# Kernel tuning notes

Hardware: AMD Instinct MI355X
Metric: run time of the kernel (lower is better)

The kernel has to match this reference:

```python
import math
import jax, jax.numpy as jnp
import numpy as np

B, N, D, E, DN, H, M = 32, 64, 256, 32, 64, 8, 32
EPS = 1e-5


def _ln(x):
    # param-free layer norm over the last axis
    mu = jnp.mean(x, axis=-1, keepdims=True)
    var = jnp.var(x, axis=-1, keepdims=True)
    return (x - mu) * jax.lax.rsqrt(var + EPS)


def setup_inputs() -> dict:
    key = jax.random.key(0)
    ks = jax.random.split(key, 9)
    embeddings = jax.random.normal(ks[0], (B, N, D), dtype=jnp.float32)
    edge_features = jax.random.normal(ks[1], (B, N, N, E), dtype=jnp.float32)
    mask = jax.random.randint(ks[2], (B, N), 0, 2).astype(bool)
    node_features = jax.random.normal(ks[3], (B, N, DN), dtype=jnp.float32)
    s = lambda d: 1.0 / math.sqrt(d)
    W_edge = jax.random.normal(ks[4], (E, H, M), dtype=jnp.float32) * s(E)
    W_recv = jax.random.normal(ks[5], (D, H, M), dtype=jnp.float32) * s(D)
    W_send = jax.random.normal(ks[6], (D, H, M), dtype=jnp.float32) * s(D)
    W_recv_node = jax.random.normal(ks[7], (DN, H, M), dtype=jnp.float32) * s(DN)
    W_send_node = jax.random.normal(ks[8], (DN, H, M), dtype=jnp.float32) * s(DN)
    return dict(embeddings=embeddings, edge_features=edge_features, mask=mask,
                node_features=node_features, W_edge=W_edge, W_recv=W_recv,
                W_send=W_send, W_recv_node=W_recv_node, W_send_node=W_send_node)


def reference(embeddings, edge_features, mask, node_features,
              W_edge, W_recv, W_send, W_recv_node, W_send_node):
    sqrt2 = math.sqrt(2.0)
    mask_f = mask.astype(embeddings.dtype)  # [B, N]
    emb = _ln(embeddings) * mask_f[..., None]  # [B, N, D]
    # double mask: [B, sender, receiver, 1]
    dm = (mask_f[..., None, :, None] * mask_f[..., :, None, None])
    ef = edge_features * dm  # [B, N, N, E]
    # projections to (heads, message_dim)
    edge_part = jnp.einsum('bije,ehm->bijhm', ef, W_edge)        # [B,N,N,H,M]
    recv = jnp.einsum('bjd,dhm->bjhm', emb, W_recv) / sqrt2      # [B,N,H,M]
    send = jnp.einsum('bid,dhm->bihm', emb, W_send) / sqrt2
    # receiver broadcast over sender axis (-4), sender over receiver axis (-3)
    rs = jnp.tanh(recv[..., None, :, :, :] + send[..., :, None, :, :])  # [B,N,N,H,M]
    rn = jnp.einsum('bjd,dhm->bjhm', node_features, W_recv_node)
    sn = jnp.einsum('bid,dhm->bihm', node_features, W_send_node)
    rs = rs * jax.nn.sigmoid((rn[..., None, :, :, :] + sn[..., :, None, :, :]) / sqrt2)
    msgs = rs * edge_part * dm[..., None]  # [B,N,N,H,M]
    updates = msgs.sum(axis=-4)            # sum over senders -> [B,N,H,M]
    updates = _ln(updates)
    return jnp.reshape(updates, (*updates.shape[:-2], -1))  # [B,N,H*M]
```

## Files before the change

kernel.cpp:

```cpp
#include <hip/hip_runtime.h>
#include <hip/hip_bf16.h>
#include <math.h>

#define B_   32
#define N_   64
#define D_   256
#define E_   32
#define DN_  64
#define H_   8
#define M_   32
#define HM_  256
#define BN_  2048
#define EPS_ 1e-5f
#define SQRT2_    1.41421356237309515f
#define NINVSQ2_ (-0.70710678118654752f)
#define MAGIC_ 0x5EEDCAFEF00DBEEFULL

typedef float f32x4 __attribute__((ext_vector_type(4)));
typedef short bf16x8 __attribute__((ext_vector_type(8)));
union U4S8 { uint4 u; bf16x8 s; };
union F2U  { float2 f; unsigned long long u; };

__device__ __forceinline__ unsigned pk2(float a, float b) {
    union { __hip_bfloat162 h; unsigned u; } cv;
    cv.h = __float22bfloat162_rn(make_float2(a, b));
    return cv.u;
}


__global__ __launch_bounds__(256, 2) void one_k(
        const float* __restrict__ emb, const float* __restrict__ edge,
        const int* __restrict__ mraw, const float* __restrict__ nfeat,
        const float* __restrict__ We, const float* __restrict__ Wr,
        const float* __restrict__ Ws, const float* __restrict__ Wrn,
        const float* __restrict__ Wsn, float* __restrict__ out,
        unsigned long long* __restrict__ g_rr,
        unsigned long long* __restrict__ g_ssC,
        unsigned long long* __restrict__ flags)
{
    const int t = threadIdx.x;
    const int w = t >> 6, l = t & 63, hi = l >> 4, lo = l & 15;
    const int blk = blockIdx.x, b = blk >> 4, s = blk & 15;
    const int j0 = s * 4;

    __shared__ int s_flag, cnt_sh;
    __shared__ unsigned long long bits_sh;
    __shared__ int sidx_s[N_];
    __shared__ __align__(16) unsigned short eln[64 * 256];
    __shared__ __align__(16) unsigned short nfs[64 * 64];
    __shared__ __align__(16) uint4 ldsA[4][256];

    if (t == 0) s_flag = 0;
    __syncthreads();
    { int v0 = mraw[t], v1 = mraw[t + 256];
      if (((v0 | v1) & ~1) != 0) atomicOr(&s_flag, 1); }
    __syncthreads();
    const bool bytef = (s_flag != 0);
    const unsigned char* mbb = (const unsigned char*)mraw;
    if (w == 0) {
        const int k = b * N_ + l;
        const bool on = bytef ? (mbb[k] != 0) : (mraw[k] != 0);
        unsigned long long bits = __ballot(on);
        if (l == 0) { bits_sh = bits; cnt_sh = __popcll(bits); }
        int p = __popcll(bits & ((1ull << l) - 1ull));
        if (on) sidx_s[p] = l;
        if (l >= __popcll(bits)) sidx_s[l] = -1;
    }
    __syncthreads();
    const unsigned long long bits = bits_sh;
    const int cb = cnt_sh;

    {
        const int mt = t >> 6, phi = (t >> 4) & 3, plo = t & 15;
        const int si = sidx_s[mt * 16 + plo];
        if (si >= 0) {
            const float* rb = edge + ((size_t)((b * N_ + si) * N_ + j0)) * E_ + phi * 8;
            #pragma unroll
            for (int q = 0; q < 4; ++q) {
                float4 v0 = *(const float4*)(rb + q * E_);
                float4 v1 = *(const float4*)(rb + q * E_ + 4);
                ldsA[q][t] = make_uint4(pk2(v0.x, v0.y), pk2(v0.z, v0.w),
                                        pk2(v1.x, v1.y), pk2(v1.z, v1.w));
            }
        } else {
            #pragma unroll
            for (int q = 0; q < 4; ++q) ldsA[q][t] = make_uint4(0, 0, 0, 0);
        }
    }

    for (int rr2 = 0; rr2 < 16; ++rr2) {
        const int i = w * 16 + rr2;
        const float mfv = ((bits >> i) & 1ull) ? 1.0f : 0.0f;
        float4 x = *(const float4*)(emb + (size_t)(b * N_ + i) * D_ + l * 4);
        float ssum = x.x + x.y + x.z + x.w;
        float s2 = x.x*x.x + x.y*x.y + x.z*x.z + x.w*x.w;
        #pragma unroll
        for (int k = 32; k >= 1; k >>= 1) { ssum += __shfl_xor(ssum, k); s2 += __shfl_xor(s2, k); }
        float mu  = ssum * (1.0f / D_);
        float var = s2 * (1.0f / D_) - mu * mu;
        float rs  = rsqrtf(var + EPS_) * mfv;
        unsigned p0 = pk2((x.x - mu) * rs, (x.y - mu) * rs);
        unsigned p1 = pk2((x.z - mu) * rs, (x.w - mu) * rs);
        unsigned off = (unsigned)(i * 512) + (((unsigned)(l * 8)) ^ (((unsigned)(i & 15)) << 4));
        *(uint2*)((char*)eln + off) = make_uint2(p0, p1);
    }
    #pragma unroll
    for (int it = 0; it < 4; ++it) {
        const int idx = it * 1024 + t * 4;
        const int r = idx >> 6, cc = idx & 63;
        float4 x = *(const float4*)(nfeat + (size_t)(b * N_ + r) * DN_ + cc);
        unsigned off = (unsigned)(r * 128) + (((unsigned)(cc * 2)) ^ (((unsigned)(r & 7)) << 4));
        *(uint2*)((char*)nfs + off) = make_uint2(pk2(x.x, x.y), pk2(x.z, x.w));
    }
    __syncthreads();

    const int nb = s * 16 + lo;
    f32x4 aR = {0,0,0,0}, aS = {0,0,0,0}, aRN = {0,0,0,0}, aSN = {0,0,0,0};
    #pragma unroll
    for (int ks = 0; ks < 8; ++ks) {
        const int i = w * 16 + lo;
        U4S8 a; a.u = *(const uint4*)((const char*)eln +
                      (unsigned)(i * 512) + (((unsigned)(ks * 64 + hi * 16)) ^ (((unsigned)(i & 15)) << 4)));
        const float* wrp = Wr + (size_t)(ks * 32 + hi * 8) * HM_ + nb;
        const float* wsp = Ws + (size_t)(ks * 32 + hi * 8) * HM_ + nb;
        U4S8 br, bs;
        br.u = make_uint4(pk2(wrp[0],     wrp[HM_]),    pk2(wrp[2*HM_], wrp[3*HM_]),
                          pk2(wrp[4*HM_], wrp[5*HM_]),  pk2(wrp[6*HM_], wrp[7*HM_]));
        bs.u = make_uint4(pk2(wsp[0],     wsp[HM_]),    pk2(wsp[2*HM_], wsp[3*HM_]),
                          pk2(wsp[4*HM_], wsp[5*HM_]),  pk2(wsp[6*HM_], wsp[7*HM_]));
        aR = __builtin_amdgcn_mfma_f32_16x16x32_bf16(a.s, br.s, aR, 0, 0, 0);
        aS = __builtin_amdgcn_mfma_f32_16x16x32_bf16(a.s, bs.s, aS, 0, 0, 0);
        if (ks < 2) {
            U4S8 a2; a2.u = *(const uint4*)((const char*)nfs +
                          (unsigned)(i * 128) + (((unsigned)(ks * 64 + hi * 16)) ^ (((unsigned)(i & 7)) << 4)));
            const float* wrn = Wrn + (size_t)(ks * 32 + hi * 8) * HM_ + nb;
            const float* wsn = Wsn + (size_t)(ks * 32 + hi * 8) * HM_ + nb;
            U4S8 brn, bsn;
            brn.u = make_uint4(pk2(wrn[0],     wrn[HM_]),   pk2(wrn[2*HM_], wrn[3*HM_]),
                               pk2(wrn[4*HM_], wrn[5*HM_]), pk2(wrn[6*HM_], wrn[7*HM_]));
            bsn.u = make_uint4(pk2(wsn[0],     wsn[HM_]),   pk2(wsn[2*HM_], wsn[3*HM_]),
                               pk2(wsn[4*HM_], wsn[5*HM_]), pk2(wsn[6*HM_], wsn[7*HM_]));
            aRN = __builtin_amdgcn_mfma_f32_16x16x32_bf16(a2.s, brn.s, aRN, 0, 0, 0);
            aSN = __builtin_amdgcn_mfma_f32_16x16x32_bf16(a2.s, bsn.s, aSN, 0, 0, 0);
        }
    }
    #pragma unroll
    for (int r = 0; r < 4; ++r) {
        const int i = w * 16 + hi * 4 + r;
        F2U rrv; rrv.f = make_float2(__expf(SQRT2_ * aR[r]), __expf(NINVSQ2_ * aRN[r]));
        __hip_atomic_store(&g_rr[(size_t)(b * N_ + i) * HM_ + nb], rrv.u,
                           __ATOMIC_RELAXED, __HIP_MEMORY_SCOPE_AGENT);
        if ((bits >> i) & 1ull) {
            const int p = __popcll(bits & ((1ull << i) - 1ull));
            F2U sv; sv.f = make_float2(__expf(SQRT2_ * aS[r]), __expf(NINVSQ2_ * aSN[r]));
            __hip_atomic_store(&g_ssC[(size_t)(b * N_ + p) * HM_ + nb], sv.u,
                               __ATOMIC_RELAXED, __HIP_MEMORY_SCOPE_AGENT);
        }
    }
    for (int p = cb + (t >> 4); p < N_; p += 16)
        __hip_atomic_store(&g_ssC[(size_t)(b * N_ + p) * HM_ + s * 16 + (t & 15)], 0ull,
                           __ATOMIC_RELAXED, __HIP_MEMORY_SCOPE_AGENT);
    __syncthreads();
    if (t == 0)
        __hip_atomic_store(&flags[b * 16 + s], MAGIC_,
                           __ATOMIC_RELEASE, __HIP_MEMORY_SCOPE_AGENT);

    if (t < 16) {
        int guard = 100000;
        while (guard-- > 0 &&
               __hip_atomic_load(&flags[b * 16 + t],
                                 __ATOMIC_ACQUIRE, __HIP_MEMORY_SCOPE_AGENT) != MAGIC_) {}
    }
    __syncthreads();

    U4S8 b4[4];
    #pragma unroll
    for (int nl = 0; nl < 4; ++nl) {
        const float* wp = We + (size_t)(hi * 8) * HM_ + w * 64 + nl * 16 + lo;
        b4[nl].u = make_uint4(pk2(wp[0],     wp[HM_]),    pk2(wp[2*HM_], wp[3*HM_]),
                              pk2(wp[4*HM_], wp[5*HM_]),  pk2(wp[6*HM_], wp[7*HM_]));
    }
    F2U rrq[4][4];
    #pragma unroll
    for (int q = 0; q < 4; ++q)
        #pragma unroll
        for (int nl = 0; nl < 4; ++nl)
            rrq[q][nl].u = __hip_atomic_load(
                &g_rr[(size_t)(b * N_ + j0 + q) * HM_ + w * 64 + nl * 16 + lo],
                __ATOMIC_RELAXED, __HIP_MEMORY_SCOPE_AGENT);

    float upd[4][4];
    #pragma unroll
    for (int q = 0; q < 4; ++q)
        #pragma unroll
        for (int nl = 0; nl < 4; ++nl) upd[q][nl] = 0.0f;

    const f32x4 zero = {0.0f, 0.0f, 0.0f, 0.0f};
    #pragma unroll
    for (int mt = 0; mt < 4; ++mt) {
        if (mt * 16 < cb) {
            F2U ssv[4][4];
            #pragma unroll
            for (int r = 0; r < 4; ++r)
                #pragma unroll
                for (int nl = 0; nl < 4; ++nl)
                    ssv[r][nl].u = __hip_atomic_load(
                        &g_ssC[(size_t)(b * N_ + mt * 16 + hi * 4 + r) * HM_ + w * 64 + nl * 16 + lo],
                        __ATOMIC_RELAXED, __HIP_MEMORY_SCOPE_AGENT);
            #pragma unroll
            for (int q = 0; q < 4; ++q) {
                if ((bits >> (j0 + q)) & 1ull) {
                    U4S8 a; a.u = ldsA[q][mt * 64 + l];
                    f32x4 acc[4];
                    #pragma unroll
                    for (int nl = 0; nl < 4; ++nl)
                        acc[nl] = __builtin_amdgcn_mfma_f32_16x16x32_bf16(a.s, b4[nl].s, zero, 0, 0, 0);
                    #pragma unroll
                    for (int r = 0; r < 4; ++r)
                        #pragma unroll
                        for (int nl = 0; nl < 4; ++nl) {
                            float u = rrq[q][nl].f.x * ssv[r][nl].f.x;
                            float v = rrq[q][nl].f.y * ssv[r][nl].f.y;
                            float den = (u + 1.0f) * (v + 1.0f);
                            float g = (u - 1.0f) * __builtin_amdgcn_rcpf(den);
                            upd[q][nl] = fmaf(g, acc[nl][r], upd[q][nl]);
                        }
                }
            }
        }
    }
    #pragma unroll
    for (int q = 0; q < 4; ++q) {
        const int j = j0 + q, bn = b * N_ + j;
        if (!((bits >> j) & 1ull)) {
            out[(size_t)bn * HM_ + w * 64 + l] = 0.0f;
            continue;
        }
        float u0 = upd[q][0], u1 = upd[q][1], u2 = upd[q][2], u3 = upd[q][3];
        u0 += __shfl_xor(u0, 16); u0 += __shfl_xor(u0, 32);
        u1 += __shfl_xor(u1, 16); u1 += __shfl_xor(u1, 32);
        u2 += __shfl_xor(u2, 16); u2 += __shfl_xor(u2, 32);
        u3 += __shfl_xor(u3, 16); u3 += __shfl_xor(u3, 32);
        float s0 = u0 + u1, q0 = u0*u0 + u1*u1;
        float s1 = u2 + u3, q1 = u2*u2 + u3*u3;
        #pragma unroll
        for (int k = 8; k >= 1; k >>= 1) {
            s0 += __shfl_xor(s0, k); q0 += __shfl_xor(q0, k);
            s1 += __shfl_xor(s1, k); q1 += __shfl_xor(q1, k);
        }
        float mu0 = s0 * (1.0f / M_), va0 = q0 * (1.0f / M_) - mu0 * mu0;
        float mu1 = s1 * (1.0f / M_), va1 = q1 * (1.0f / M_) - mu1 * mu1;
        float rs0 = rsqrtf(va0 + EPS_), rs1 = rsqrtf(va1 + EPS_);
        float v01 = (hi & 1) ? u1 : u0;
        float v23 = (hi & 1) ? u3 : u2;
        float val = (hi < 2) ? v01 : v23;
        float o = (hi < 2) ? (val - mu0) * rs0 : (val - mu1) * rs1;
        out[(size_t)bn * HM_ + w * 64 + l] = o;
    }
}

extern "C" void kernel_launch(void* const* d_in, const int* in_sizes, int n_in,
                              void* d_out, int out_size, void* d_ws, size_t ws_size,
                              hipStream_t stream) {
    const float* embeddings = (const float*)d_in[0];
    const float* edge_feat  = (const float*)d_in[1];
    const int*   mask_raw   = (const int*)d_in[2];
    const float* node_feat  = (const float*)d_in[3];
    const float* W_edge     = (const float*)d_in[4];
    const float* W_recv     = (const float*)d_in[5];
    const float* W_send     = (const float*)d_in[6];
    const float* W_recvn    = (const float*)d_in[7];
    const float* W_sendn    = (const float*)d_in[8];
    float* out = (float*)d_out;

    unsigned long long* g_ssC = (unsigned long long*)d_ws;
    unsigned long long* g_rr  = g_ssC + (size_t)BN_ * HM_;
    unsigned long long* flags = g_rr + (size_t)BN_ * HM_;

    one_k<<<512, 256, 0, stream>>>(embeddings, edge_feat, mask_raw, node_feat,
                                   W_edge, W_recv, W_send, W_recvn, W_sendn,
                                   out, g_rr, g_ssC, flags);
}
```

Measured before the change: 41.82 us.

## Split fused kernel into node and edge kernels, drop flag spin-wait

Replaces the single fused kernel, which used inter-block spin-waiting on global flags, with two launches. The node kernel computes the projections, applies layer norm directly from registers without staging in LDS, and writes through plain stores instead of atomics. The edge kernel consumes those results after the launch boundary and exits early when all four receivers in its tile are masked. It also remaps blocks by XCD so each batch's blocks share an L2, adds an occupancy hint of 4, and trims LDS use; the cost is a second launch and its gap.

```diff
diff --git a/kernel.cpp b/kernel.cpp
--- a/kernel.cpp
+++ b/kernel.cpp
@@ -14,12 +14,10 @@
 #define EPS_ 1e-5f
 #define SQRT2_    1.41421356237309515f
 #define NINVSQ2_ (-0.70710678118654752f)
-#define MAGIC_ 0x5EEDCAFEF00DBEEFULL
 
 typedef float f32x4 __attribute__((ext_vector_type(4)));
 typedef short bf16x8 __attribute__((ext_vector_type(8)));
 union U4S8 { uint4 u; bf16x8 s; };
-union F2U  { float2 f; unsigned long long u; };
 
 __device__ __forceinline__ unsigned pk2(float a, float b) {
     union { __hip_bfloat162 h; unsigned u; } cv;
@@ -28,47 +26,153 @@
 }
 
 
-__global__ __launch_bounds__(256, 2) void one_k(
-        const float* __restrict__ emb, const float* __restrict__ edge,
-        const int* __restrict__ mraw, const float* __restrict__ nfeat,
-        const float* __restrict__ We, const float* __restrict__ Wr,
-        const float* __restrict__ Ws, const float* __restrict__ Wrn,
-        const float* __restrict__ Wsn, float* __restrict__ out,
-        unsigned long long* __restrict__ g_rr,
-        unsigned long long* __restrict__ g_ssC,
-        unsigned long long* __restrict__ flags)
-{
-    const int t = threadIdx.x;
-    const int w = t >> 6, l = t & 63, hi = l >> 4, lo = l & 15;
-    const int blk = blockIdx.x, b = blk >> 4, s = blk & 15;
-    const int j0 = s * 4;
-
-    __shared__ int s_flag, cnt_sh;
-    __shared__ unsigned long long bits_sh;
-    __shared__ int sidx_s[N_];
-    __shared__ __align__(16) unsigned short eln[64 * 256];
-    __shared__ __align__(16) unsigned short nfs[64 * 64];
-    __shared__ __align__(16) uint4 ldsA[4][256];
-
-    if (t == 0) s_flag = 0;
+__device__ __forceinline__ void remap(int wg, int& b, int& s) {
+    const int xcd = wg & 7;
+    b = xcd * 4 + (wg >> 7);
+    s = (wg >> 3) & 15;
+}
+
+__device__ __forceinline__ unsigned long long mask_bits(
+        const int* mraw, int b, int t, int w, int l, int* s_flag_sh,
+        unsigned long long* bits_sh) {
+    if (t == 0) *s_flag_sh = 0;
     __syncthreads();
     { int v0 = mraw[t], v1 = mraw[t + 256];
-      if (((v0 | v1) & ~1) != 0) atomicOr(&s_flag, 1); }
-    __syncthreads();
-    const bool bytef = (s_flag != 0);
+      if (((v0 | v1) & ~1) != 0) atomicOr(s_flag_sh, 1); }
+    __syncthreads();
+    const bool bytef = (*s_flag_sh != 0);
     const unsigned char* mbb = (const unsigned char*)mraw;
     if (w == 0) {
         const int k = b * N_ + l;
         const bool on = bytef ? (mbb[k] != 0) : (mraw[k] != 0);
         unsigned long long bits = __ballot(on);
-        if (l == 0) { bits_sh = bits; cnt_sh = __popcll(bits); }
+        if (l == 0) *bits_sh = bits;
+    }
+    __syncthreads();
+    return *bits_sh;
+}
+
+__global__ __launch_bounds__(256, 4) void node_k(
+        const float* __restrict__ emb, const float* __restrict__ nfeat,
+        const int* __restrict__ mraw,
+        const float* __restrict__ Wr, const float* __restrict__ Ws,
+        const float* __restrict__ Wrn, const float* __restrict__ Wsn,
+        float2* __restrict__ g_rr, float2* __restrict__ g_ssC) {
+    const int t = threadIdx.x;
+    const int w = t >> 6, l = t & 63, hi = l >> 4, lo = l & 15;
+    int b, s; remap(blockIdx.x, b, s);
+
+    __shared__ int s_flag;
+    __shared__ unsigned long long bits_sh;
+    const unsigned long long bits = mask_bits(mraw, b, t, w, l, &s_flag, &bits_sh);
+    const int cb = __popcll(bits);
+
+    float mu_l, rs_l;
+    {
+        const int qrow = w * 16 + (l >> 2);
+        const float* rp = emb + (size_t)(b * N_ + qrow) * D_ + (l & 3) * 64;
+        float sv = 0.f, s2 = 0.f;
+        #pragma unroll
+        for (int k = 0; k < 16; ++k) {
+            float4 x = *(const float4*)(rp + k * 4);
+            sv += x.x + x.y + x.z + x.w;
+            s2 += x.x*x.x + x.y*x.y + x.z*x.z + x.w*x.w;
+        }
+        sv += __shfl_xor(sv, 1); sv += __shfl_xor(sv, 2);
+        s2 += __shfl_xor(s2, 1); s2 += __shfl_xor(s2, 2);
+        float mu  = sv * (1.0f / D_);
+        float var = s2 * (1.0f / D_) - mu * mu;
+        float rs  = rsqrtf(var + EPS_) * (((bits >> qrow) & 1ull) ? 1.0f : 0.0f);
+        mu_l = __shfl(mu, lo << 2);
+        rs_l = __shfl(rs, lo << 2);
+    }
+
+    const int nb = s * 16 + lo;
+    const float* arow = emb   + (size_t)(b * N_ + w * 16 + lo) * D_  + hi * 8;
+    const float* nrow = nfeat + (size_t)(b * N_ + w * 16 + lo) * DN_ + hi * 8;
+    f32x4 aR = {0,0,0,0}, aS = {0,0,0,0}, aRN = {0,0,0,0}, aSN = {0,0,0,0};
+    #pragma unroll
+    for (int ks = 0; ks < 8; ++ks) {
+        float4 xa = *(const float4*)(arow + ks * 32);
+        float4 xb = *(const float4*)(arow + ks * 32 + 4);
+        U4S8 a;
+        a.u = make_uint4(pk2((xa.x - mu_l) * rs_l, (xa.y - mu_l) * rs_l),
+                         pk2((xa.z - mu_l) * rs_l, (xa.w - mu_l) * rs_l),
+                         pk2((xb.x - mu_l) * rs_l, (xb.y - mu_l) * rs_l),
+                         pk2((xb.z - mu_l) * rs_l, (xb.w - mu_l) * rs_l));
+        const float* wrp = Wr + (size_t)(ks * 32 + hi * 8) * HM_ + nb;
+        const float* wsp = Ws + (size_t)(ks * 32 + hi * 8) * HM_ + nb;
+        U4S8 br, bs;
+        br.u = make_uint4(pk2(wrp[0],     wrp[HM_]),    pk2(wrp[2*HM_], wrp[3*HM_]),
+                          pk2(wrp[4*HM_], wrp[5*HM_]),  pk2(wrp[6*HM_], wrp[7*HM_]));
+        bs.u = make_uint4(pk2(wsp[0],     wsp[HM_]),    pk2(wsp[2*HM_], wsp[3*HM_]),
+                          pk2(wsp[4*HM_], wsp[5*HM_]),  pk2(wsp[6*HM_], wsp[7*HM_]));
+        aR = __builtin_amdgcn_mfma_f32_16x16x32_bf16(a.s, br.s, aR, 0, 0, 0);
+        aS = __builtin_amdgcn_mfma_f32_16x16x32_bf16(a.s, bs.s, aS, 0, 0, 0);
+        if (ks < 2) {
+            float4 na = *(const float4*)(nrow + ks * 32);
+            float4 nb4 = *(const float4*)(nrow + ks * 32 + 4);
+            U4S8 a2;
+            a2.u = make_uint4(pk2(na.x, na.y),  pk2(na.z, na.w),
+                              pk2(nb4.x, nb4.y), pk2(nb4.z, nb4.w));
+            const float* wrn = Wrn + (size_t)(ks * 32 + hi * 8) * HM_ + nb;
+            const float* wsn = Wsn + (size_t)(ks * 32 + hi * 8) * HM_ + nb;
+            U4S8 brn, bsn;
+            brn.u = make_uint4(pk2(wrn[0],     wrn[HM_]),   pk2(wrn[2*HM_], wrn[3*HM_]),
+                               pk2(wrn[4*HM_], wrn[5*HM_]), pk2(wrn[6*HM_], wrn[7*HM_]));
+            bsn.u = make_uint4(pk2(wsn[0],     wsn[HM_]),   pk2(wsn[2*HM_], wsn[3*HM_]),
+                               pk2(wsn[4*HM_], wsn[5*HM_]), pk2(wsn[6*HM_], wsn[7*HM_]));
+            aRN = __builtin_amdgcn_mfma_f32_16x16x32_bf16(a2.s, brn.s, aRN, 0, 0, 0);
+            aSN = __builtin_amdgcn_mfma_f32_16x16x32_bf16(a2.s, bsn.s, aSN, 0, 0, 0);
+        }
+    }
+
+    #pragma unroll
+    for (int r = 0; r < 4; ++r) {
+        const int i = w * 16 + hi * 4 + r;
+        g_rr[(size_t)(b * N_ + i) * HM_ + nb] =
+            make_float2(__expf(SQRT2_ * aR[r]), __expf(NINVSQ2_ * aRN[r]));
+        if ((bits >> i) & 1ull) {
+            const int p = __popcll(bits & ((1ull << i) - 1ull));
+            g_ssC[(size_t)(b * N_ + p) * HM_ + nb] =
+                make_float2(__expf(SQRT2_ * aS[r]), __expf(NINVSQ2_ * aSN[r]));
+        }
+    }
+    for (int p = cb + (t >> 4); p < N_; p += 16)
+        g_ssC[(size_t)(b * N_ + p) * HM_ + s * 16 + (t & 15)] = make_float2(0.f, 0.f);
+}
+
+__global__ __launch_bounds__(256, 4) void edge_k(
+        const float* __restrict__ edge, const float* __restrict__ We,
+        const int* __restrict__ mraw,
+        const float2* __restrict__ g_rr, const float2* __restrict__ g_ssC,
+        float* __restrict__ out) {
+    const int t = threadIdx.x;
+    const int w = t >> 6, l = t & 63, hi = l >> 4, lo = l & 15;
+    int b, s; remap(blockIdx.x, b, s);
+    const int j0 = s * 4;
+
+    __shared__ int s_flag;
+    __shared__ unsigned long long bits_sh;
+    __shared__ int sidx_s[N_];
+    __shared__ __align__(16) uint4 ldsA[4][256];
+
+    const unsigned long long bits = mask_bits(mraw, b, t, w, l, &s_flag, &bits_sh);
+    const int cb = __popcll(bits);
+    if (w == 0) {
+        const bool on = (bits >> l) & 1ull;
         int p = __popcll(bits & ((1ull << l) - 1ull));
         if (on) sidx_s[p] = l;
-        if (l >= __popcll(bits)) sidx_s[l] = -1;
-    }
-    __syncthreads();
-    const unsigned long long bits = bits_sh;
-    const int cb = cnt_sh;
+        if (l >= cb) sidx_s[l] = -1;
+    }
+    __syncthreads();
+
+    if (((bits >> j0) & 15ull) == 0ull) {
+        #pragma unroll
+        for (int q = 0; q < 4; ++q)
+            out[(size_t)(b * N_ + j0 + q) * HM_ + t] = 0.0f;
+        return;
+    }
 
     {
         const int mt = t >> 6, phi = (t >> 4) & 3, plo = t & 15;
@@ -87,90 +191,6 @@
             for (int q = 0; q < 4; ++q) ldsA[q][t] = make_uint4(0, 0, 0, 0);
         }
     }
-
-    for (int rr2 = 0; rr2 < 16; ++rr2) {
-        const int i = w * 16 + rr2;
-        const float mfv = ((bits >> i) & 1ull) ? 1.0f : 0.0f;
-        float4 x = *(const float4*)(emb + (size_t)(b * N_ + i) * D_ + l * 4);
-        float ssum = x.x + x.y + x.z + x.w;
-        float s2 = x.x*x.x + x.y*x.y + x.z*x.z + x.w*x.w;
-        #pragma unroll
-        for (int k = 32; k >= 1; k >>= 1) { ssum += __shfl_xor(ssum, k); s2 += __shfl_xor(s2, k); }
-        float mu  = ssum * (1.0f / D_);
-        float var = s2 * (1.0f / D_) - mu * mu;
-        float rs  = rsqrtf(var + EPS_) * mfv;
-        unsigned p0 = pk2((x.x - mu) * rs, (x.y - mu) * rs);
-        unsigned p1 = pk2((x.z - mu) * rs, (x.w - mu) * rs);
-        unsigned off = (unsigned)(i * 512) + (((unsigned)(l * 8)) ^ (((unsigned)(i & 15)) << 4));
-        *(uint2*)((char*)eln + off) = make_uint2(p0, p1);
-    }
-    #pragma unroll
-    for (int it = 0; it < 4; ++it) {
-        const int idx = it * 1024 + t * 4;
-        const int r = idx >> 6, cc = idx & 63;
-        float4 x = *(const float4*)(nfeat + (size_t)(b * N_ + r) * DN_ + cc);
-        unsigned off = (unsigned)(r * 128) + (((unsigned)(cc * 2)) ^ (((unsigned)(r & 7)) << 4));
-        *(uint2*)((char*)nfs + off) = make_uint2(pk2(x.x, x.y), pk2(x.z, x.w));
-    }
-    __syncthreads();
-
-    const int nb = s * 16 + lo;
-    f32x4 aR = {0,0,0,0}, aS = {0,0,0,0}, aRN = {0,0,0,0}, aSN = {0,0,0,0};
-    #pragma unroll
-    for (int ks = 0; ks < 8; ++ks) {
-        const int i = w * 16 + lo;
-        U4S8 a; a.u = *(const uint4*)((const char*)eln +
-                      (unsigned)(i * 512) + (((unsigned)(ks * 64 + hi * 16)) ^ (((unsigned)(i & 15)) << 4)));
-        const float* wrp = Wr + (size_t)(ks * 32 + hi * 8) * HM_ + nb;
-        const float* wsp = Ws + (size_t)(ks * 32 + hi * 8) * HM_ + nb;
-        U4S8 br, bs;
-        br.u = make_uint4(pk2(wrp[0],     wrp[HM_]),    pk2(wrp[2*HM_], wrp[3*HM_]),
-                          pk2(wrp[4*HM_], wrp[5*HM_]),  pk2(wrp[6*HM_], wrp[7*HM_]));
-        bs.u = make_uint4(pk2(wsp[0],     wsp[HM_]),    pk2(wsp[2*HM_], wsp[3*HM_]),
-                          pk2(wsp[4*HM_], wsp[5*HM_]),  pk2(wsp[6*HM_], wsp[7*HM_]));
-        aR = __builtin_amdgcn_mfma_f32_16x16x32_bf16(a.s, br.s, aR, 0, 0, 0);
-        aS = __builtin_amdgcn_mfma_f32_16x16x32_bf16(a.s, bs.s, aS, 0, 0, 0);
-        if (ks < 2) {
-            U4S8 a2; a2.u = *(const uint4*)((const char*)nfs +
-                          (unsigned)(i * 128) + (((unsigned)(ks * 64 + hi * 16)) ^ (((unsigned)(i & 7)) << 4)));
-            const float* wrn = Wrn + (size_t)(ks * 32 + hi * 8) * HM_ + nb;
-            const float* wsn = Wsn + (size_t)(ks * 32 + hi * 8) * HM_ + nb;
-            U4S8 brn, bsn;
-            brn.u = make_uint4(pk2(wrn[0],     wrn[HM_]),   pk2(wrn[2*HM_], wrn[3*HM_]),
-                               pk2(wrn[4*HM_], wrn[5*HM_]), pk2(wrn[6*HM_], wrn[7*HM_]));
-            bsn.u = make_uint4(pk2(wsn[0],     wsn[HM_]),   pk2(wsn[2*HM_], wsn[3*HM_]),
-                               pk2(wsn[4*HM_], wsn[5*HM_]), pk2(wsn[6*HM_], wsn[7*HM_]));
-            aRN = __builtin_amdgcn_mfma_f32_16x16x32_bf16(a2.s, brn.s, aRN, 0, 0, 0);
-            aSN = __builtin_amdgcn_mfma_f32_16x16x32_bf16(a2.s, bsn.s, aSN, 0, 0, 0);
-        }
-    }
-    #pragma unroll
-    for (int r = 0; r < 4; ++r) {
-        const int i = w * 16 + hi * 4 + r;
-        F2U rrv; rrv.f = make_float2(__expf(SQRT2_ * aR[r]), __expf(NINVSQ2_ * aRN[r]));
-        __hip_atomic_store(&g_rr[(size_t)(b * N_ + i) * HM_ + nb], rrv.u,
-                           __ATOMIC_RELAXED, __HIP_MEMORY_SCOPE_AGENT);
-        if ((bits >> i) & 1ull) {
-            const int p = __popcll(bits & ((1ull << i) - 1ull));
-            F2U sv; sv.f = make_float2(__expf(SQRT2_ * aS[r]), __expf(NINVSQ2_ * aSN[r]));
-            __hip_atomic_store(&g_ssC[(size_t)(b * N_ + p) * HM_ + nb], sv.u,
-                               __ATOMIC_RELAXED, __HIP_MEMORY_SCOPE_AGENT);
-        }
-    }
-    for (int p = cb + (t >> 4); p < N_; p += 16)
-        __hip_atomic_store(&g_ssC[(size_t)(b * N_ + p) * HM_ + s * 16 + (t & 15)], 0ull,
-                           __ATOMIC_RELAXED, __HIP_MEMORY_SCOPE_AGENT);
-    __syncthreads();
-    if (t == 0)
-        __hip_atomic_store(&flags[b * 16 + s], MAGIC_,
-                           __ATOMIC_RELEASE, __HIP_MEMORY_SCOPE_AGENT);
-
-    if (t < 16) {
-        int guard = 100000;
-        while (guard-- > 0 &&
-               __hip_atomic_load(&flags[b * 16 + t],
-                                 __ATOMIC_ACQUIRE, __HIP_MEMORY_SCOPE_AGENT) != MAGIC_) {}
-    }
     __syncthreads();
 
     U4S8 b4[4];
@@ -180,14 +200,13 @@
         b4[nl].u = make_uint4(pk2(wp[0],     wp[HM_]),    pk2(wp[2*HM_], wp[3*HM_]),
                               pk2(wp[4*HM_], wp[5*HM_]),  pk2(wp[6*HM_], wp[7*HM_]));
     }
-    F2U rrq[4][4];
+
+    float2 rrq[4][4];
     #pragma unroll
     for (int q = 0; q < 4; ++q)
         #pragma unroll
         for (int nl = 0; nl < 4; ++nl)
-            rrq[q][nl].u = __hip_atomic_load(
-                &g_rr[(size_t)(b * N_ + j0 + q) * HM_ + w * 64 + nl * 16 + lo],
-                __ATOMIC_RELAXED, __HIP_MEMORY_SCOPE_AGENT);
+            rrq[q][nl] = g_rr[(size_t)(b * N_ + j0 + q) * HM_ + w * 64 + nl * 16 + lo];
 
     float upd[4][4];
     #pragma unroll
@@ -199,14 +218,14 @@
     #pragma unroll
     for (int mt = 0; mt < 4; ++mt) {
         if (mt * 16 < cb) {
-            F2U ssv[4][4];
+            float2 ssv[4][4];
             #pragma unroll
-            for (int r = 0; r < 4; ++r)
+            for (int r = 0; r < 4; ++r) {
+                const float2* srow =
+                    g_ssC + (size_t)(b * N_ + mt * 16 + hi * 4 + r) * HM_ + w * 64 + lo;
                 #pragma unroll
-                for (int nl = 0; nl < 4; ++nl)
-                    ssv[r][nl].u = __hip_atomic_load(
-                        &g_ssC[(size_t)(b * N_ + mt * 16 + hi * 4 + r) * HM_ + w * 64 + nl * 16 + lo],
-                        __ATOMIC_RELAXED, __HIP_MEMORY_SCOPE_AGENT);
+                for (int nl = 0; nl < 4; ++nl) ssv[r][nl] = srow[nl * 16];
+            }
             #pragma unroll
             for (int q = 0; q < 4; ++q) {
                 if ((bits >> (j0 + q)) & 1ull) {
@@ -219,8 +238,8 @@
                     for (int r = 0; r < 4; ++r)
                         #pragma unroll
                         for (int nl = 0; nl < 4; ++nl) {
-                            float u = rrq[q][nl].f.x * ssv[r][nl].f.x;
-                            float v = rrq[q][nl].f.y * ssv[r][nl].f.y;
+                            float u = rrq[q][nl].x * ssv[r][nl].x;
+                            float v = rrq[q][nl].y * ssv[r][nl].y;
                             float den = (u + 1.0f) * (v + 1.0f);
                             float g = (u - 1.0f) * __builtin_amdgcn_rcpf(den);
                             upd[q][nl] = fmaf(g, acc[nl][r], upd[q][nl]);
@@ -273,11 +292,12 @@
     const float* W_sendn    = (const float*)d_in[8];
     float* out = (float*)d_out;
 
-    unsigned long long* g_ssC = (unsigned long long*)d_ws;
-    unsigned long long* g_rr  = g_ssC + (size_t)BN_ * HM_;
-    unsigned long long* flags = g_rr + (size_t)BN_ * HM_;
-
-    one_k<<<512, 256, 0, stream>>>(embeddings, edge_feat, mask_raw, node_feat,
-                                   W_edge, W_recv, W_send, W_recvn, W_sendn,
-                                   out, g_rr, g_ssC, flags);
-}
+    float2* g_ssC = (float2*)d_ws;
+    float2* g_rr  = g_ssC + (size_t)BN_ * HM_;
+
+    node_k<<<512, 256, 0, stream>>>(embeddings, node_feat, mask_raw,
+                                    W_recv, W_send, W_recvn, W_sendn,
+                                    g_rr, g_ssC);
+    edge_k<<<512, 256, 0, stream>>>(edge_feat, W_edge, mask_raw,
+                                    g_rr, g_ssC, out);
+}
```

Result: no change. 41.27 us (-1.3%).
